# Kernel tuning notes

Hardware: AMD Instinct MI355X
Metric: run time of the kernel (lower is better)

Reference implementation:

```python
import jax, jax.numpy as jnp
import numpy as np

GATE_SLOPE = 5.0
BRANCH_BREAK = 0.5

def setup_inputs() -> dict:
    key = jax.random.key(0)
    ks = jax.random.split(key, 6)
    B, I, O, N = 1024, 64, 64, 16
    x = jax.random.normal(ks[0], (B, I), dtype=jnp.float32)
    k = jax.random.uniform(ks[1], (I, O, N), dtype=jnp.float32) * 2 + 0.5
    Ec = jax.random.uniform(ks[2], (I, O, N), dtype=jnp.float32) * 2 + 0.5
    Ps = jax.random.uniform(ks[3], (I, O, N), dtype=jnp.float32) * 1.5 + 0.5
    bias = jax.random.normal(ks[4], (I, O, N), dtype=jnp.float32) * 0.1
    coef = jax.random.normal(ks[5], (I, O, N), dtype=jnp.float32)
    return {"x": x, "k": k, "Ec": Ec, "Ps": Ps, "bias": bias, "coef": coef}

def reference(x, k, Ec, Ps, bias, coef):
    # prev_x buffer starts at zeros and is overwritten (detached) with the
    # previous sample each loop iteration -> prev row = shifted x.
    prev = jnp.concatenate([jnp.zeros((1, x.shape[1]), x.dtype), x[:-1]], axis=0)
    dx = x - jax.lax.stop_gradient(prev)                  # (B, I)
    g = jax.nn.sigmoid(GATE_SLOPE * dx)
    branch = (g > BRANCH_BREAK).astype(x.dtype)[:, :, None, None]  # (B, I, 1, 1)
    xe = x[:, :, None, None]                              # (B, I, 1, 1)
    # Ps * (2*sigmoid(k*(x -/+ Ec)) - 1)
    P_up = Ps * (2.0 * jax.nn.sigmoid(k * (xe - Ec)) - 1.0)   # (B, I, O, N)
    P_down = Ps * (2.0 * jax.nn.sigmoid(k * (xe + Ec)) - 1.0)
    basis = branch * P_up + (1.0 - branch) * P_down + bias
    # weighted sum over in_dim and num_basis -> (B, O)
    return jnp.einsum('bion,ion->bo', basis, coef)
```

## Files before the change

kernel.cpp:

```cpp
#include <hip/hip_runtime.h>
#include <hip/hip_bf16.h>


#define LOG2E 1.44269504088896340736f
#define B_DIM 1024
#define I_DIM 64
#define O_DIM 64
#define N_DIM 16
#define ION   65536

__device__ __forceinline__ float ex2(float x) {
#if __has_builtin(__builtin_amdgcn_exp2f)
  return __builtin_amdgcn_exp2f(x);
#else
  return exp2f(x);
#endif
}

__global__ __launch_bounds__(256) void prep(
    const float* __restrict__ k, const float* __restrict__ Ec,
    const float* __restrict__ Ps, const float* __restrict__ bias,
    const float* __restrict__ coef, float4* __restrict__ Q,
    float* __restrict__ Wsum) {
  int idx = blockIdx.x * 256 + threadIdx.x;
  int i = idx >> 10, o = (idx >> 4) & 63, n = idx & 15;
  float kv = k[idx], ev = Ec[idx], pv = Ps[idx], bv = bias[idx], cv = coef[idx];
  float kk = -LOG2E * kv;
  float E  =  LOG2E * kv * ev;
  float A  =  2.0f * pv * cv;
  float W  = (bv - pv) * cv;
  Q[(i * N_DIM + n) * O_DIM + o] = make_float4(kk, E, A, 0.0f);
  #pragma unroll
  for (int off = 1; off < 16; off <<= 1)
    W += __shfl_xor(W, off, 64);
  if (n == 0) Wsum[i * O_DIM + o] = W;
}

__global__ __launch_bounds__(256) void ferro_main(
    const float* __restrict__ x, const float4* __restrict__ Q,
    const float* __restrict__ Wsum, float* __restrict__ part) {
  int t  = threadIdx.x;
  int o  = t & 63;
  int w  = t >> 6;
  int ic = blockIdx.x & 15;
  int bc = blockIdx.x >> 4;
  int r0 = bc * 32 + w * 8;

  float acc[8];
  #pragma unroll
  for (int j = 0; j < 8; ++j) acc[j] = 0.0f;
  float wadd = 0.0f;

  #pragma unroll 1
  for (int ii = 0; ii < 4; ++ii) {
    int i = ic * 4 + ii;
    wadd += Wsum[i * O_DIM + o];
    float xv[9];
    xv[0] = (r0 == 0) ? 0.0f : x[(r0 - 1) * I_DIM + i];
    #pragma unroll
    for (int j = 0; j < 8; ++j) xv[j + 1] = x[(r0 + j) * I_DIM + i];
    bool br[8];
    #pragma unroll
    for (int j = 0; j < 8; ++j) br[j] = xv[j + 1] > xv[j];

    const float4* q = Q + (i * N_DIM) * O_DIM + o;
    #pragma unroll
    for (int n = 0; n < N_DIM; ++n) {
      float4 p = q[n * O_DIM];
      float E = p.y, nE = -p.y;
      #pragma unroll
      for (int j = 0; j < 8; ++j) {
        float e = br[j] ? E : nE;
        float z = fmaf(p.x, xv[j + 1], e);
        float s = __builtin_amdgcn_rcpf(1.0f + ex2(z));
        acc[j] = fmaf(p.z, s, acc[j]);
      }
    }
  }

  float* dst = part + ((size_t)ic * B_DIM + r0) * O_DIM + o;
  #pragma unroll
  for (int j = 0; j < 8; ++j)
    dst[j * O_DIM] = acc[j] + wadd;
}

__global__ __launch_bounds__(256) void reduce_k(
    const float* __restrict__ part, float* __restrict__ out) {
  int gid = blockIdx.x * 256 + threadIdx.x;
  float s = 0.f;
  #pragma unroll
  for (int ic = 0; ic < 16; ++ic) s += part[ic * (B_DIM * O_DIM) + gid];
  out[gid] = s;
}

extern "C" void kernel_launch(void* const* d_in, const int* in_sizes, int n_in,
                              void* d_out, int out_size, void* d_ws, size_t ws_size,
                              hipStream_t stream) {
  const float* x    = (const float*)d_in[0];
  const float* k    = (const float*)d_in[1];
  const float* Ec   = (const float*)d_in[2];
  const float* Ps   = (const float*)d_in[3];
  const float* bias = (const float*)d_in[4];
  const float* coef = (const float*)d_in[5];
  float* out = (float*)d_out;

  float4* Q    = (float4*)d_ws;
  float*  Wsum = (float*)((char*)d_ws + (size_t)ION * sizeof(float4));
  float*  part = (float*)((char*)Wsum + (size_t)I_DIM * O_DIM * sizeof(float));

  hipLaunchKernelGGL(prep,       dim3(ION / 256), dim3(256), 0, stream,
                     k, Ec, Ps, bias, coef, Q, Wsum);
  hipLaunchKernelGGL(ferro_main, dim3(512),       dim3(256), 0, stream,
                     x, Q, Wsum, part);
  hipLaunchKernelGGL(reduce_k,   dim3(B_DIM * O_DIM / 256), dim3(256), 0, stream,
                     part, out);
}
```

Baseline: 83.26 us.

## Fuse parameter preprocessing into main kernel using shared-memory staging

Removes the separate prep kernel. Each block now converts the k/Ec/Ps/bias/coef slice for its four input channels into float4 coefficients, including the bias-weight term, and stages them in 64KB of LDS. The main loop reads the coefficients from LDS instead of a global workspace. This saves one launch and the global Q/Wsum round trip, but each parameter slice is recomputed by the 32 blocks sharing an ic, and the 64KB of LDS may limit occupancy.

```diff
diff --git a/kernel.cpp b/kernel.cpp
--- a/kernel.cpp
+++ b/kernel.cpp
@@ -7,7 +7,6 @@
 #define I_DIM 64
 #define O_DIM 64
 #define N_DIM 16
-#define ION   65536
 
 __device__ __forceinline__ float ex2(float x) {
 #if __has_builtin(__builtin_amdgcn_exp2f)
@@ -17,44 +16,45 @@
 #endif
 }
 
-__global__ __launch_bounds__(256) void prep(
-    const float* __restrict__ k, const float* __restrict__ Ec,
-    const float* __restrict__ Ps, const float* __restrict__ bias,
-    const float* __restrict__ coef, float4* __restrict__ Q,
-    float* __restrict__ Wsum) {
-  int idx = blockIdx.x * 256 + threadIdx.x;
-  int i = idx >> 10, o = (idx >> 4) & 63, n = idx & 15;
-  float kv = k[idx], ev = Ec[idx], pv = Ps[idx], bv = bias[idx], cv = coef[idx];
-  float kk = -LOG2E * kv;
-  float E  =  LOG2E * kv * ev;
-  float A  =  2.0f * pv * cv;
-  float W  = (bv - pv) * cv;
-  Q[(i * N_DIM + n) * O_DIM + o] = make_float4(kk, E, A, 0.0f);
-  #pragma unroll
-  for (int off = 1; off < 16; off <<= 1)
-    W += __shfl_xor(W, off, 64);
-  if (n == 0) Wsum[i * O_DIM + o] = W;
-}
+__global__ __launch_bounds__(256) void ferro_fused(
+    const float* __restrict__ x, const float* __restrict__ k,
+    const float* __restrict__ Ec, const float* __restrict__ Ps,
+    const float* __restrict__ bias, const float* __restrict__ coef,
+    float* __restrict__ part) {
+  __shared__ float4 Qs[4 * N_DIM * O_DIM];
 
-__global__ __launch_bounds__(256) void ferro_main(
-    const float* __restrict__ x, const float4* __restrict__ Q,
-    const float* __restrict__ Wsum, float* __restrict__ part) {
   int t  = threadIdx.x;
   int o  = t & 63;
   int w  = t >> 6;
   int ic = blockIdx.x & 15;
   int bc = blockIdx.x >> 4;
+
+  #pragma unroll
+  for (int j = 0; j < 16; ++j) {
+    int e   = t + j * 256;
+    int il  = e >> 10;
+    int rem = e & 1023;
+    int oo  = rem >> 4, n = rem & 15;
+    int g   = (ic * 4 + il) * 1024 + rem;
+    float kv = k[g], ev = Ec[g], pv = Ps[g], bv = bias[g], cv = coef[g];
+    float kk = -LOG2E * kv;
+    float E  =  LOG2E * kv * ev;
+    float A  =  2.0f * pv * cv;
+    float W  = (bv - pv) * cv;
+    Qs[(il * N_DIM + n) * O_DIM + oo] = make_float4(kk, E, A, W);
+  }
+  __syncthreads();
+
   int r0 = bc * 32 + w * 8;
 
   float acc[8];
   #pragma unroll
   for (int j = 0; j < 8; ++j) acc[j] = 0.0f;
-  float wadd = 0.0f;
+  float wsum = 0.0f;
 
   #pragma unroll 1
-  for (int ii = 0; ii < 4; ++ii) {
-    int i = ic * 4 + ii;
-    wadd += Wsum[i * O_DIM + o];
+  for (int il = 0; il < 4; ++il) {
+    int i = ic * 4 + il;
     float xv[9];
     xv[0] = (r0 == 0) ? 0.0f : x[(r0 - 1) * I_DIM + i];
     #pragma unroll
@@ -63,11 +63,12 @@
     #pragma unroll
     for (int j = 0; j < 8; ++j) br[j] = xv[j + 1] > xv[j];
 
-    const float4* q = Q + (i * N_DIM) * O_DIM + o;
+    const float4* q = &Qs[(il * N_DIM) * O_DIM + o];
     #pragma unroll
     for (int n = 0; n < N_DIM; ++n) {
       float4 p = q[n * O_DIM];
       float E = p.y, nE = -p.y;
+      wsum += p.w;
       #pragma unroll
       for (int j = 0; j < 8; ++j) {
         float e = br[j] ? E : nE;
@@ -81,7 +82,7 @@
   float* dst = part + ((size_t)ic * B_DIM + r0) * O_DIM + o;
   #pragma unroll
   for (int j = 0; j < 8; ++j)
-    dst[j * O_DIM] = acc[j] + wadd;
+    dst[j * O_DIM] = acc[j] + wsum;
 }
 
 __global__ __launch_bounds__(256) void reduce_k(
@@ -104,14 +105,10 @@
   const float* coef = (const float*)d_in[5];
   float* out = (float*)d_out;
 
-  float4* Q    = (float4*)d_ws;
-  float*  Wsum = (float*)((char*)d_ws + (size_t)ION * sizeof(float4));
-  float*  part = (float*)((char*)Wsum + (size_t)I_DIM * O_DIM * sizeof(float));
+  float* part = (float*)d_ws;
 
-  hipLaunchKernelGGL(prep,       dim3(ION / 256), dim3(256), 0, stream,
-                     k, Ec, Ps, bias, coef, Q, Wsum);
-  hipLaunchKernelGGL(ferro_main, dim3(512),       dim3(256), 0, stream,
-                     x, Q, Wsum, part);
-  hipLaunchKernelGGL(reduce_k,   dim3(B_DIM * O_DIM / 256), dim3(256), 0, stream,
+  hipLaunchKernelGGL(ferro_fused, dim3(512), dim3(256), 0, stream,
+                     x, k, Ec, Ps, bias, coef, part);
+  hipLaunchKernelGGL(reduce_k, dim3(B_DIM * O_DIM / 256), dim3(256), 0, stream,
                      part, out);
 }
```

Result: no change. 83.99 us (+0.9%).
